# Kernel optimization log

Measured on AMD Instinct MI355X. Metric: run time of the kernel, lower is better.

Reference implementation:

```python
import jax, jax.numpy as jnp
import numpy as np

B, LQ, LT, LC = 256, 50, 12, 60
S = LQ + LT + LC
T = 80
D = 512   # gnn_hidden = lstm_hidden = att_vec_size
A = 128   # action_embed_size
FD = 64   # field_embed_size
TD = 64   # type_embed_size
NH = 8
DH = D // NH
NPROD, NFIELD, NTYPE = 96, 60, 30
IN_DIM = A + D + A + FD + TD + D  # prev_action|context|parent_prod|parent_field|parent_type|parent_state


def setup_inputs() -> dict:
    ks = jax.random.split(jax.random.key(0), 40)
    it = iter(range(40))
    def nrm(shape, scale=0.05):
        return jax.random.normal(ks[next(it)], shape, jnp.float32) * scale
    inp = {}
    inp["encodings"] = jax.random.normal(ks[next(it)], (B, S, D), jnp.float32)
    inp["mask"] = jnp.ones((B, S), dtype=bool)
    inp["h0"] = jax.random.normal(ks[next(it)], (B, D), jnp.float32)
    inp["act_type"] = jax.random.randint(ks[next(it)], (T, B), 0, 4)
    inp["act_idx"] = jax.random.randint(ks[next(it)], (T, B), 0, LT)
    inp["action_len"] = jax.random.randint(ks[next(it)], (B,), 1, T + 1)
    inp["parent_t"] = jax.random.randint(ks[next(it)], (T, B), 0, T)
    inp["frontier_prod"] = jax.random.randint(ks[next(it)], (T, B), 0, NPROD)
    inp["frontier_field"] = jax.random.randint(ks[next(it)], (T, B), 0, NFIELD)
    inp["frontier_type"] = jax.random.randint(ks[next(it)], (T, B), 0, NTYPE)
    inp["prod_embed"] = nrm((NPROD + 1, A))
    inp["field_embed"] = nrm((NFIELD, FD))
    inp["type_embed"] = nrm((NTYPE, TD))
    inp["col_in_W"] = nrm((D, A))
    inp["col_in_b"] = jnp.zeros((A,), jnp.float32)
    inp["lstm_Wi"] = nrm((IN_DIM, 4 * D))
    inp["lstm_Wh"] = nrm((D, 4 * D))
    inp["lstm_b"] = jnp.zeros((4 * D,), jnp.float32)
    for name in ("ctx", "colattn", "tabattn"):
        for w in ("Wq", "Wk", "Wv", "Wo"):
            inp[f"{name}_{w}"] = nrm((D, D))
    inp["att_W"] = nrm((2 * D, D))
    inp["att_b"] = jnp.zeros((D,), jnp.float32)
    inp["rule_W"] = nrm((D, A))
    return inp


def _mha(mem, m, q, Wq, Wk, Wv, Wo):
    # mem: [B,S,D] keys/values, q: [B,D] single-step query, m: [B,S] valid mask
    Sm = mem.shape[1]
    qh = (q @ Wq).reshape(B, NH, DH)
    kh = (mem @ Wk).reshape(B, Sm, NH, DH)
    vh = (mem @ Wv).reshape(B, Sm, NH, DH)
    scores = jnp.einsum('bhd,bshd->bhs', qh, kh) * (1.0 / float(np.sqrt(DH)))
    scores = jnp.where(m[:, None, :], scores, -1e9)
    p = jax.nn.softmax(scores, axis=-1)                  # [B,NH,S]
    ctx = jnp.einsum('bhs,bshd->bhd', p, vh).reshape(B, D) @ Wo
    return ctx, p.mean(axis=1)                           # context, head-avg attn prob


def forward(encodings, mask, h0, act_type, act_idx, action_len, parent_t,
            frontier_prod, frontier_field, frontier_type,
            prod_embed, field_embed, type_embed, col_in_W, col_in_b,
            lstm_Wi, lstm_Wh, lstm_b,
            ctx_Wq, ctx_Wk, ctx_Wv, ctx_Wo, att_W, att_b, rule_W,
            colattn_Wq, colattn_Wk, colattn_Wv, colattn_Wo,
            tabattn_Wq, tabattn_Wk, tabattn_Wv, tabattn_Wo):
    tab = encodings[:, LQ:LQ + LT]
    col = encodings[:, LQ + LT:]
    tab_mask = mask[:, LQ:LQ + LT]
    col_mask = mask[:, LQ + LT:]
    bidx = jnp.arange(B)

    def lstm_step(x, h, c):
        g = x @ lstm_Wi + h @ lstm_Wh + lstm_b
        i, f, gg, o = jnp.split(g, 4, axis=-1)
        c2 = jax.nn.sigmoid(f) * c + jax.nn.sigmoid(i) * jnp.tanh(gg)
        h2 = jax.nn.sigmoid(o) * jnp.tanh(c2)
        return h2, c2

    def decode_step(x, h, c):
        h2, c2 = lstm_step(x, h, c)
        ctx, _ = _mha(encodings, mask, h2, ctx_Wq, ctx_Wk, ctx_Wv, ctx_Wo)
        att = jnp.tanh(jnp.concatenate([h2, ctx], axis=-1) @ att_W + att_b)
        rule_lp = jax.nn.log_softmax((att @ rule_W) @ prod_embed.T, axis=-1)   # [B, NPROD+1]
        _, colp = _mha(col, col_mask, att, colattn_Wq, colattn_Wk, colattn_Wv, colattn_Wo)
        _, tabp = _mha(tab, tab_mask, att, tabattn_Wq, tabattn_Wk, tabattn_Wv, tabattn_Wo)
        return h2, c2, ctx, rule_lp, jnp.log(colp + 1e-32), jnp.log(tabp + 1e-32)

    def gather_lp(rule_lp, col_lp, tab_lp, atype, aidx):
        lp_rule = rule_lp[bidx, aidx]
        return jnp.where(atype == 0, lp_rule,
               jnp.where(atype == 1, rule_lp[:, NPROD],
               jnp.where(atype == 2, col_lp[bidx, aidx], tab_lp[bidx, aidx])))

    # ---- step t = 0: context from h0, zero input except context + root-type embed ----
    ctx0, _ = _mha(encodings, mask, h0, ctx_Wq, ctx_Wk, ctx_Wv, ctx_Wo)
    x0 = jnp.zeros((B, IN_DIM), encodings.dtype)
    x0 = x0.at[:, A:A + D].set(ctx0)
    off = A + D + A + FD
    x0 = x0.at[:, off:off + TD].set(jnp.broadcast_to(type_embed[0], (B, TD)))
    h, c, ctx, rule_lp, col_lp, tab_lp = decode_step(x0, h0, jnp.zeros_like(h0))
    lp0 = gather_lp(rule_lp, col_lp, tab_lp, act_type[0], act_idx[0])
    loss = jnp.sum(jnp.where(action_len > 0, lp0, 0.0))
    history = jnp.zeros((T, B, D), encodings.dtype).at[0].set(h)

    # ---- steps t = 1..T-1 ----
    def step(carry, xs):
        h, c, ctx, history, loss = carry
        t, ptype, pidx, atype, aidx, par, fp, ff, ft = xs
        valid = t < action_len                              # [B]
        # prev action embedding, gathered by heterogeneous action type
        pe_rule = prod_embed[jnp.where(ptype == 1, NPROD, pidx)]
        col_e = col[bidx, pidx] @ col_in_W + col_in_b
        tab_e = tab[bidx, pidx] @ col_in_W + col_in_b       # table_lstm_input shares weights
        prev = jnp.where((ptype <= 1)[:, None], pe_rule,
               jnp.where((ptype == 2)[:, None], col_e, tab_e))
        prev = jnp.where(valid[:, None], prev, 0.0)
        par_eff = jnp.where(valid, jnp.minimum(par, t - 1), 0)
        parent_state = history[par_eff, bidx]               # [B,D]
        x = jnp.concatenate([prev, ctx, prod_embed[fp], field_embed[ff],
                             type_embed[ft], parent_state], axis=-1)
        h, c, ctx, rule_lp, col_lp, tab_lp = decode_step(x, h, c)
        lp = gather_lp(rule_lp, col_lp, tab_lp, atype, aidx)
        loss = loss + jnp.sum(jnp.where(valid, lp, 0.0))
        history = jax.lax.dynamic_update_index_in_dim(history, h, t, 0)
        return (h, c, ctx, history, loss), None

    xs = (jnp.arange(1, T), act_type[:-1], act_idx[:-1], act_type[1:], act_idx[1:],
          parent_t[1:], frontier_prod[1:], frontier_field[1:], frontier_type[1:])
    (h, c, ctx, history, loss), _ = jax.lax.scan(step, (h, c, ctx, history, loss), xs)
    return -loss


def reference(encodings, mask, h0, act_type, act_idx, action_len, parent_t,
              frontier_prod, frontier_field, frontier_type,
              prod_embed, field_embed, type_embed, col_in_W, col_in_b,
              lstm_Wi, lstm_Wh, lstm_b,
              ctx_Wq, ctx_Wk, ctx_Wv, ctx_Wo, att_W, att_b, rule_W,
              colattn_Wq, colattn_Wk, colattn_Wv, colattn_Wo,
              tabattn_Wq, tabattn_Wk, tabattn_Wv, tabattn_Wo):
    return forward(encodings, mask, h0, act_type, act_idx, action_len, parent_t,
                   frontier_prod, frontier_field, frontier_type,
                   prod_embed, field_embed, type_embed, col_in_W, col_in_b,
                   lstm_Wi, lstm_Wh, lstm_b,
                   ctx_Wq, ctx_Wk, ctx_Wv, ctx_Wo, att_W, att_b, rule_W,
                   colattn_Wq, colattn_Wk, colattn_Wv, colattn_Wo,
                   tabattn_Wq, tabattn_Wk, tabattn_Wv, tabattn_Wo)
```

## Files before the change

### kernel.cpp

```cpp
#include <hip/hip_runtime.h>

typedef unsigned short u16;
typedef unsigned char u8;
typedef __attribute__((ext_vector_type(8))) short bf16x8;
typedef __attribute__((ext_vector_type(4))) float f32x4;
typedef __attribute__((ext_vector_type(2))) float f32x2;

#define NB   256
#define SEQ  122
#define TLT  12
#define TLC  60
#define NTT  80
#define DD   512
#define IND  1408
#define XHD  1920

__device__ __forceinline__ float bf2f(u16 u){ union{unsigned int i; float f;} x; x.i = ((unsigned int)u)<<16u; return x.f; }
__device__ __forceinline__ u16 f2bf(float f){ union{float f; unsigned int i;} x; x.f=f; unsigned int r = x.i + 0x7fffu + ((x.i>>16)&1u); return (u16)(r>>16); }

__device__ __forceinline__ void gstore(float* p, float v){ *p = v; }
__device__ __forceinline__ void gstore(u16* p, float v){ *p = f2bf(v); }

__global__ __launch_bounds__(256) void convert_bf16(const float* __restrict__ in, u16* __restrict__ out, int n){
    for (int i = blockIdx.x*256 + threadIdx.x; i < n; i += gridDim.x*256) out[i] = f2bf(in[i]);
// ... 43 lines not shown
    __shared__ float tile[64][65];
    int k0 = blockIdx.y*64, n0 = blockIdx.x*64;
    int c = threadIdx.x & 63, r4 = threadIdx.x >> 6;
    #pragma unroll
    for (int i = 0; i < 16; i++){
        int r = r4 + i*4;
        tile[r][c] = in[(size_t)(k0+r)*N + n0 + c];
    }
    __syncthreads();
    #pragma unroll
    for (int i = 0; i < 16; i++){
        int n = n0 + r4 + i*4;
        int pn = (n & 511)*4 + (n >> 9);
        out[(size_t)pn*ldo + koff + k0 + c] = f2bf(tile[c][r4 + i*4]);
    }
}

template<typename TOUT, int ACT>
__global__ __launch_bounds__(256) void gemm_kernel(
    const u16* __restrict__ Abase, int lda, int rpb, int sb, int aoff,
    const u16* __restrict__ BT,
    TOUT* __restrict__ C, int ldc,
    u16* __restrict__ C2, int ldc2,
    const float* __restrict__ bias, int K)
{
    __shared__ u16 As[64*40];
    __shared__ u16 Bs[64*40];
    const int bn = blockIdx.x * 64;
    const int bm = blockIdx.y * 64;
    const int tid = threadIdx.x, lane = tid & 63, wid = tid >> 6;
    const int wr = wid >> 1, wc = wid & 1;
    f32x4 acc[2][2];
    #pragma unroll
    for (int i=0;i<2;i++)
      #pragma unroll
      for (int j=0;j<2;j++) acc[i][j] = (f32x4){0.f,0.f,0.f,0.f};

    const int srow = tid >> 2, sseg = (tid & 3) << 3;
    int ar = bm + srow;
    int abr = (ar / rpb) * sb + aoff + (ar % rpb);
    const u16* ap = Abase + (size_t)abr * lda + sseg;
    const u16* bp = BT + (size_t)(bn + srow) * K + sseg;
    const int frow = lane & 15, fk = (lane >> 4) << 3;

    for (int k0 = 0; k0 < K; k0 += 32){
        uint4 av = *(const uint4*)(ap + k0);
        uint4 bv = *(const uint4*)(bp + k0);
        __syncthreads();
        *(uint4*)(&As[srow*40 + sseg]) = av;
        *(uint4*)(&Bs[srow*40 + sseg]) = bv;
        __syncthreads();
        #pragma unroll
        for (int i = 0; i < 2; i++){
            bf16x8 afr = *reinterpret_cast<const bf16x8*>(&As[(wr*32 + i*16 + frow)*40 + fk]);
            #pragma unroll
            for (int j = 0; j < 2; j++){
                bf16x8 bfr = *reinterpret_cast<const bf16x8*>(&Bs[(wc*32 + j*16 + frow)*40 + fk]);
                acc[i][j] = __builtin_amdgcn_mfma_f32_16x16x32_bf16(afr, bfr, acc[i][j], 0, 0, 0);
            }
        }
    }
    const int crow = (lane >> 4) * 4, ccol = lane & 15;
    #pragma unroll
    for (int i = 0; i < 2; i++){
        #pragma unroll
        for (int j = 0; j < 2; j++){
            int col = bn + wc*32 + j*16 + ccol;
            float bval = bias ? bias[col] : 0.0f;
            #pragma unroll
            for (int r = 0; r < 4; r++){
                int row = bm + wr*32 + i*16 + crow + r;
                float v = acc[i][j][r] + bval;
                if (ACT == 1) v = tanhf(v);
                gstore(&C[(size_t)row*ldc + col], v);
                if (C2) C2[(size_t)row*ldc2 + col] = f2bf(v);
            }
        }
    }
}

__global__ __launch_bounds__(256) void convert_h0(const float* __restrict__ h0, u16* __restrict__ hcP, u16* __restrict__ xh){
    int idx = blockIdx.x*256 + threadIdx.x;
    int b = idx >> 9, d = idx & 511;
    u16 hb = f2bf(h0[idx]);
    hcP[(size_t)b*1024 + d] = hb;
    xh[(size_t)b*XHD + IND + d] = hb;
}

__global__ __launch_bounds__(256) void build_x0(const float* __restrict__ typeE, u16* __restrict__ xh, float* __restrict__ cbuf){
    int b = blockIdx.x, tid = threadIdx.x;
    u16* xr = xh + (size_t)b*XHD;
    for (int j = tid; j < IND; j += 256){
        float v = (j >= 832 && j < 896) ? typeE[j-832] : 0.f;
        xr[j] = f2bf(v);
    }
    for (int j = tid; j < 512; j += 256) cbuf[(size_t)b*512 + j] = 0.f;
}

__global__ __launch_bounds__(256) void reduce_loss(const float* __restrict__ lp, float* __restrict__ out){
    __shared__ float sh[256];
    float s = 0.f;
    for (int i = threadIdx.x; i < NTT*NB; i += 256) s += lp[i];
    sh[threadIdx.x] = s; __syncthreads();
    for (int st = 128; st > 0; st >>= 1){ if (threadIdx.x < st) sh[threadIdx.x] += sh[threadIdx.x+st]; __syncthreads(); }
    if (threadIdx.x == 0) out[0] = -sh[0];
}


__device__ __forceinline__ void gemm64(const u16* __restrict__ A0, int lda,
                                       const u16* __restrict__ B0, int ldb,
                                       int K, u16* As, u16* Bs, f32x4 (&acc)[2][2])
{
    const int tid = threadIdx.x, lane = tid & 63;
    const int wid = tid >> 6, wr = wid >> 1, wc = wid & 1;
    const int frow = lane & 15, fk = (lane >> 4) << 3;
    const int srow = tid >> 2, sk = (tid & 3) << 4;
    const u16* ap = A0 + (size_t)srow * lda + sk;
    const u16* bp = B0 + (size_t)srow * ldb + sk;
    uint4 a0 = *(const uint4*)ap, a1 = *(const uint4*)(ap + 8);
    uint4 b0 = *(const uint4*)bp, b1 = *(const uint4*)(bp + 8);
    for (int k0 = 0; k0 < K; k0 += 64){
        __syncthreads();
        *(uint4*)&As[srow*72 + sk]     = a0;
        *(uint4*)&As[srow*72 + sk + 8] = a1;
        *(uint4*)&Bs[srow*72 + sk]     = b0;
        *(uint4*)&Bs[srow*72 + sk + 8] = b1;
        __syncthreads();
        if (k0 + 64 < K){
            ap += 64; bp += 64;
            a0 = *(const uint4*)ap; a1 = *(const uint4*)(ap + 8);
            b0 = *(const uint4*)bp; b1 = *(const uint4*)(bp + 8);
        }
        #pragma unroll
        for (int ks = 0; ks < 2; ks++){
            bf16x8 af0 = *(const bf16x8*)&As[(wr*32 + frow)*72      + ks*32 + fk];
            bf16x8 af1 = *(const bf16x8*)&As[(wr*32 + 16 + frow)*72 + ks*32 + fk];
            bf16x8 bf0 = *(const bf16x8*)&Bs[(wc*32 + frow)*72      + ks*32 + fk];
            bf16x8 bf1 = *(const bf16x8*)&Bs[(wc*32 + 16 + frow)*72 + ks*32 + fk];
            acc[0][0] = __builtin_amdgcn_mfma_f32_16x16x32_bf16(af0, bf0, acc[0][0], 0,0,0);
            acc[0][1] = __builtin_amdgcn_mfma_f32_16x16x32_bf16(af0, bf1, acc[0][1], 0,0,0);
            acc[1][0] = __builtin_amdgcn_mfma_f32_16x16x32_bf16(af1, bf0, acc[1][0], 0,0,0);
            acc[1][1] = __builtin_amdgcn_mfma_f32_16x16x32_bf16(af1, bf1, acc[1][1], 0,0,0);
        }
    }
}

__device__ __forceinline__ void zacc(f32x4 (&acc)[2][2]){
    #pragma unroll
    for (int i=0;i<2;i++)
      #pragma unroll
      for (int j=0;j<2;j++) acc[i][j] = (f32x4){0.f,0.f,0.f,0.f};
}

__global__ __launch_bounds__(256) void gates_lstm(
    int t, const u16* __restrict__ xh, const u16* __restrict__ WcatTp,
    const float* __restrict__ lb, float* __restrict__ cbuf,
    u16* __restrict__ hc)
{
    __shared__ union { struct { u16 A[2][32*72]; u16 B[2][32*72]; } g; float ep[32*33]; } sm;
    const int nt = blockIdx.x, mt = blockIdx.y;
    const int tid = threadIdx.x, lane = tid & 63, wid = tid >> 6;
    const int wr = wid >> 1, wc = wid & 1;
    const int frow = lane & 15, fk = (lane >> 4) << 3;
    const int crow = (lane >> 4) << 2, ccol = lane & 15;
    f32x4 acc = (f32x4){0.f,0.f,0.f,0.f};
    {
        const int srow = tid >> 2, sk = (tid & 3) << 4;
        const bool isA = srow < 32;
        const int drow = isA ? srow : srow - 32;
        const u16* p = isA ? (xh + (size_t)(mt*32 + srow)*XHD + sk)
                           : (WcatTp + (size_t)(nt*32 + (srow - 32))*XHD + sk);
        uint4 a0 = *(const uint4*)p, a1 = *(const uint4*)(p + 8);
        {
            u16* d = isA ? &sm.g.A[0][drow*72 + sk] : &sm.g.B[0][drow*72 + sk];
            *(uint4*)d = a0; *(uint4*)(d + 8) = a1;
        }
        __syncthreads();
        const int NIT = XHD/64;
        for (int i = 0; i < NIT; i++){
            if (i + 1 < NIT){
                p += 64;
                a0 = *(const uint4*)p; a1 = *(const uint4*)(p + 8);
            }
            const int cur = i & 1;
            #pragma unroll
            for (int ks = 0; ks < 2; ks++){
                bf16x8 af = *(const bf16x8*)&sm.g.A[cur][(wr*16 + frow)*72 + ks*32 + fk];
                bf16x8 bf = *(const bf16x8*)&sm.g.B[cur][(wc*16 + frow)*72 + ks*32 + fk];
                acc = __builtin_amdgcn_mfma_f32_16x16x32_bf16(af, bf, acc, 0,0,0);
            }
            if (i + 1 < NIT){
                u16* d = isA ? &sm.g.A[cur^1][drow*72 + sk] : &sm.g.B[cur^1][drow*72 + sk];
                *(uint4*)d = a0; *(uint4*)(d + 8) = a1;
                __syncthreads();
            }
        }
    }
    __syncthreads();
    #pragma unroll
    for (int r = 0; r < 4; r++)
        sm.ep[(wr*16 + crow + r)*33 + wc*16 + ccol] = acc[r];
    __syncthreads();
    {
        const int bloc = tid >> 3, dl = tid & 7;
        const int b = mt*32 + bloc, d = nt*8 + dl;
        float iv = sm.ep[bloc*33 + dl*4 + 0] + lb[d];
        float fv = sm.ep[bloc*33 + dl*4 + 1] + lb[512 + d];
        float gv = sm.ep[bloc*33 + dl*4 + 2] + lb[1024 + d];
        float ov = sm.ep[bloc*33 + dl*4 + 3] + lb[1536 + d];
        float c  = cbuf[(size_t)b*512 + d];
        float si = 1.f/(1.f + __expf(-iv));
        float sf = 1.f/(1.f + __expf(-fv));
        float so = 1.f/(1.f + __expf(-ov));
        float c2 = sf*c + si*tanhf(gv);
        float h2 = so*tanhf(c2);
        cbuf[(size_t)b*512 + d] = c2;
        hc[((size_t)t*NB + b)*1024 + d] = f2bf(h2);
    }
}

template<int ACT>
__global__ __launch_bounds__(256) void step_gemm(
    const u16* __restrict__ A0, int lda,
    const u16* __restrict__ BT, int ldb, int K,
    u16* __restrict__ C, int ldc, u16* __restrict__ C2, int ldc2,
    const float* __restrict__ bias)
{
    __shared__ u16 As[64*72];
    __shared__ u16 Bs[64*72];
    const int nt = blockIdx.x, mt = blockIdx.y;
    const int tid = threadIdx.x, lane = tid & 63, wid = tid >> 6;
    const int wr = wid >> 1, wc = wid & 1;
    const int crow = (lane >> 4) << 2, ccol = lane & 15;
    f32x4 acc[2][2]; zacc(acc);
    gemm64(A0 + (size_t)(mt*64)*lda, lda, BT + (size_t)(nt*64)*ldb, ldb, K, As, Bs, acc);
    #pragma unroll
    for (int i = 0; i < 2; i++)
      #pragma unroll
      for (int j = 0; j < 2; j++){
        int col = nt*64 + wc*32 + j*16 + ccol;
        float bv = bias ? bias[col] : 0.f;
        #pragma unroll
        for (int r = 0; r < 4; r++){
            int b = mt*64 + wr*32 + i*16 + crow + r;
            float v = acc[i][j][r] + bv;
            if (ACT == 1) v = tanhf(v);
            u16 hb = f2bf(v);
            C[(size_t)b*ldc + col] = hb;
            if (C2) C2[(size_t)b*ldc2 + col] = hb;
        }
      }
}

__device__ __forceinline__ float dot8(uint4 v, const float qv[8]){
    float a = 0.f;
    a += qv[0]*bf2f((u16)(v.x & 0xffffu)); a += qv[1]*bf2f((u16)(v.x >> 16));
    a += qv[2]*bf2f((u16)(v.y & 0xffffu)); a += qv[3]*bf2f((u16)(v.y >> 16));
    a += qv[4]*bf2f((u16)(v.z & 0xffffu)); a += qv[5]*bf2f((u16)(v.z >> 16));
    a += qv[6]*bf2f((u16)(v.w & 0xffffu)); a += qv[7]*bf2f((u16)(v.w >> 16));
    return a;
}

__device__ __forceinline__ float dot8f8(uint2 w, const float qv[8]){
    f32x2 a0 = __builtin_amdgcn_cvt_pk_f32_fp8((int)w.x, false);
    f32x2 a1 = __builtin_amdgcn_cvt_pk_f32_fp8((int)w.x, true);
    f32x2 a2 = __builtin_amdgcn_cvt_pk_f32_fp8((int)w.y, false);
    f32x2 a3 = __builtin_amdgcn_cvt_pk_f32_fp8((int)w.y, true);
    return qv[0]*a0.x + qv[1]*a0.y + qv[2]*a1.x + qv[3]*a1.y
         + qv[4]*a2.x + qv[5]*a2.y + qv[6]*a3.x + qv[7]*a3.y;
}
__device__ __forceinline__ void fma8f8(uint2 w, float pw, float a8[8]){
    f32x2 a0 = __builtin_amdgcn_cvt_pk_f32_fp8((int)w.x, false);
    f32x2 a1 = __builtin_amdgcn_cvt_pk_f32_fp8((int)w.x, true);
    f32x2 a2 = __builtin_amdgcn_cvt_pk_f32_fp8((int)w.y, false);
    f32x2 a3 = __builtin_amdgcn_cvt_pk_f32_fp8((int)w.y, true);
    a8[0] += pw*a0.x; a8[1] += pw*a0.y; a8[2] += pw*a1.x; a8[3] += pw*a1.y;
    a8[4] += pw*a2.x; a8[5] += pw*a2.y; a8[6] += pw*a3.x; a8[7] += pw*a3.y;
}

__global__ __launch_bounds__(512) void attnq_kernel(
    int t, const u16* __restrict__ WqTc, const u8* __restrict__ K8, const u8* __restrict__ V8,
    u16* __restrict__ hc_t, u16* __restrict__ xh,
    const u16* __restrict__ hc,
    const float* __restrict__ prodE, const float* __restrict__ fieldE, const float* __restrict__ typeE,
    const u16* __restrict__ cole, const u16* __restrict__ tabe,
    const int* __restrict__ act_type, const int* __restrict__ act_idx, const int* __restrict__ action_len,
    const int* __restrict__ parent_t, const int* __restrict__ f_prod, const int* __restrict__ f_field,
    const int* __restrict__ f_type)
{
    const int h = blockIdx.x, g = blockIdx.y;
    const int gb0 = g*8;
    const int tid = threadIdx.x;
    __shared__ u16 As2[2][16*72];
    __shared__ u16 Bs2[2][64*72];
    __shared__ float qs2[2][16*64];
    __shared__ float qs[16*64];
    __shared__ float sc[8*124];
    __shared__ float part[8*8*64];
    {
        const int kg = tid >> 8;
        const int lt = tid & 255;
        const int lane = lt & 63, wid4 = lt >> 6;
        const int frow = lane & 15, fk = (lane >> 4) << 3;
        f32x4 acc = (f32x4){0.f,0.f,0.f,0.f};
        const int srow = lt >> 2, sk = (lt & 3) << 4;
        const bool al = lt < 32;
        const u16* ap = hc_t + (size_t)(gb0 + srow)*1024 + kg*256 + sk;
        const u16* bp = WqTc + (size_t)(h*64 + srow)*512 + kg*256 + sk;
        u16* Ag = As2[kg]; u16* Bg = Bs2[kg];
        uint4 a0, a1, b0, b1;
        if (al){ a0 = *(const uint4*)ap; a1 = *(const uint4*)(ap + 8); }
        b0 = *(const uint4*)bp; b1 = *(const uint4*)(bp + 8);
        for (int k0 = 0; k0 < 256; k0 += 64){
            __syncthreads();
            if (al){ *(uint4*)&Ag[srow*72 + sk] = a0; *(uint4*)&Ag[srow*72 + sk + 8] = a1; }
            *(uint4*)&Bg[srow*72 + sk] = b0; *(uint4*)&Bg[srow*72 + sk + 8] = b1;
            __syncthreads();
            if (k0 + 64 < 256){
                bp += 64; b0 = *(const uint4*)bp; b1 = *(const uint4*)(bp + 8);
                if (al){ ap += 64; a0 = *(const uint4*)ap; a1 = *(const uint4*)(ap + 8); }
            }
            #pragma unroll
            for (int ks = 0; ks < 2; ks++){
                bf16x8 af = *(const bf16x8*)&Ag[frow*72 + ks*32 + fk];
                bf16x8 bf = *(const bf16x8*)&Bg[(wid4*16 + frow)*72 + ks*32 + fk];
                acc = __builtin_amdgcn_mfma_f32_16x16x32_bf16(af, bf, acc, 0,0,0);
            }
        }
        __syncthreads();
        #pragma unroll
        for (int r = 0; r < 4; r++)
            qs2[kg][((lane>>4)*4 + r)*64 + wid4*16 + (lane & 15)] = acc[r];
    }
    __syncthreads();
    for (int i = tid; i < 1024; i += 512)
        qs[i] = (qs2[0][i] + qs2[1][i]) * 0.125f;
    __syncthreads();
    {
        const int gi = tid >> 3, l8 = tid & 7;
        const int bq = gi & 7, sq = gi >> 3;
        float q8[8];
        const float* qrow = qs + bq*64 + l8*8;
        #pragma unroll
        for (int e = 0; e < 8; e++) q8[e] = qrow[e];
        const u8* Kb = K8 + ((size_t)(gb0 + bq)*SEQ)*512 + h*64 + l8*8;
        #pragma unroll 4
        for (int k = 0; k < 16; k++){
            int s = sq*16 + k;
            if (s < SEQ){
                uint2 kw = *(const uint2*)(Kb + (size_t)s*512);
                float a = dot8f8(kw, q8);
                a += __shfl_xor(a, 1); a += __shfl_xor(a, 2); a += __shfl_xor(a, 4);
                if (l8 == 0) sc[bq*124 + s] = a;
            }
        }
    }
    __syncthreads();
    {
        const int bq = tid >> 6, lid = tid & 63;
        float* scr = sc + bq*124;
        float m = -1e30f;
        for (int s = lid; s < SEQ; s += 64) m = fmaxf(m, scr[s]);
        #pragma unroll
        for (int mm = 1; mm < 64; mm <<= 1) m = fmaxf(m, __shfl_xor(m, mm));
        float sum = 0.f;
        for (int s = lid; s < SEQ; s += 64){ float e = __expf(scr[s] - m); scr[s] = e; sum += e; }
        #pragma unroll
        for (int mm = 1; mm < 64; mm <<= 1) sum += __shfl_xor(sum, mm);
        float inv = 1.f/sum;
        for (int s = lid; s < SEQ; s += 64) scr[s] *= inv;
    }
    __syncthreads();
    {
        const int gi = tid >> 3, l8 = tid & 7;
        const int bq = gi & 7, sq = gi >> 3;
        float a8[8] = {0.f,0.f,0.f,0.f,0.f,0.f,0.f,0.f};
        const u8* Vb = V8 + ((size_t)(gb0 + bq)*SEQ)*512 + h*64 + l8*8;
        const float* pr = sc + bq*124;
        #pragma unroll 4
        for (int k = 0; k < 16; k++){
            int s = sq*16 + k;
            if (s < SEQ){
                uint2 vw = *(const uint2*)(Vb + (size_t)s*512);
                fma8f8(vw, pr[s], a8);
            }
        }
        #pragma unroll
        for (int e = 0; e < 8; e++) part[(sq*8 + bq)*64 + l8*8 + e] = a8[e];
    }
    __syncthreads();
    if (tid < 256){
        const int bq = tid >> 5, d0 = (tid & 31)*2;
        float v0 = 0.f, v1 = 0.f;
        #pragma unroll
        for (int sq = 0; sq < 8; sq++){
            v0 += part[(sq*8 + bq)*64 + d0];
            v1 += part[(sq*8 + bq)*64 + d0 + 1];
        }
        unsigned outw = ((unsigned)f2bf(v1) << 16) | (unsigned)f2bf(v0);
        int b = gb0 + bq, c0 = h*64 + d0;
        *(unsigned*)(hc_t + (size_t)b*1024 + 512 + c0) = outw;
        *(unsigned*)(xh + (size_t)b*XHD + 128 + c0) = outw;
    }
    if (t >= 0 && t + 1 < NTT){
        int tn = t + 1;
        int b = gb0 + h;
        u16* xr = xh + (size_t)b*XHD;
        bool validn = tn < action_len[b];
        int ptype = act_type[t*NB + b], pidx = act_idx[t*NB + b];
        int fp = f_prod[tn*NB + b], ff = f_field[tn*NB + b], ftp = f_type[tn*NB + b];
        int par = parent_t[tn*NB + b];
        int pe = validn ? min(par, t) : 0;
        const u16* hrow  = hc + ((size_t)pe*NB + b)*1024;
        const u16* h2row = hc_t + (size_t)b*1024;
        if (tid < 256){
            unsigned v1 = *(const unsigned*)(hrow + tid*2);
            unsigned v2 = *(const unsigned*)(h2row + tid*2);
            *(unsigned*)(xr + 896 + tid*2)  = v1;
            *(unsigned*)(xr + 1408 + tid*2) = v2;
        } else if (tid < 384){
            int j = tid - 256;
            float v;
            if (!validn) v = 0.f;
            else if (ptype <= 1) v = prodE[(ptype == 1 ? 96 : pidx)*128 + j];
            else if (ptype == 2) v = bf2f(cole[((size_t)b*TLC + pidx)*128 + j]);
            else                 v = bf2f(tabe[((size_t)b*TLT + pidx)*128 + j]);
            xr[j] = f2bf(v);
            xr[640 + j] = f2bf(prodE[fp*128 + j]);
        } else if (tid < 448){
            int j = tid - 384;
            xr[768 + j] = f2bf(fieldE[ff*64 + j]);
            xr[832 + j] = f2bf(typeE[ftp*64 + j]);
        }
    }
}

__global__ __launch_bounds__(256) void tail_lp(
    const u16* __restrict__ rcq_all, const u16* __restrict__ Kcol, const u16* __restrict__ Ktab,
    const int* __restrict__ act_type, const int* __restrict__ act_idx, const int* __restrict__ action_len,
    float* __restrict__ lp_buf)
{
    const int t = blockIdx.x, b = blockIdx.y;
    const int tid = threadIdx.x;
    __shared__ float qc[512], qt[512];
    __shared__ float sccc[8*65];
    __shared__ float scct[8*17];
    __shared__ float lg[100];
    __shared__ float colv[64];
    __shared__ float tabv[16];
    __shared__ float red2[4];
    const u16* row = rcq_all + ((size_t)t*NB + b)*1152;
    if (tid < 97) lg[tid] = bf2f(row[tid]);
    {
        unsigned v = *(const unsigned*)(row + 128 + tid*2);
        qc[tid*2]   = bf2f((u16)(v & 0xffffu))*0.125f;
        qc[tid*2+1] = bf2f((u16)(v >> 16))*0.125f;
        unsigned v2 = *(const unsigned*)(row + 640 + tid*2);
        qt[tid*2]   = bf2f((u16)(v2 & 0xffffu))*0.125f;
        qt[tid*2+1] = bf2f((u16)(v2 >> 16))*0.125f;
    }
    __syncthreads();
    {
        const int gi = tid >> 3, l8 = tid & 7;
        for (int u = gi; u < 640; u += 32){
            if (u < 512){
                int hh = u >> 6, s = u & 63;
                if (s < TLC){
                    uint4 kv = *(const uint4*)(Kcol + ((size_t)b*TLC + s)*512 + hh*64 + l8*8);
                    float qv[8];
                    #pragma unroll
                    for (int e = 0; e < 8; e++) qv[e] = qc[hh*64 + l8*8 + e];
                    float a = dot8(kv, qv);
                    a += __shfl_xor(a, 1); a += __shfl_xor(a, 2); a += __shfl_xor(a, 4);
                    if (l8 == 0) sccc[hh*65 + s] = a;
                }
            } else {
                int v = u - 512, hh = v >> 4, s = v & 15;
                if (s < TLT){
                    uint4 kv = *(const uint4*)(Ktab + ((size_t)b*TLT + s)*512 + hh*64 + l8*8);
                    float qv[8];
                    #pragma unroll
                    for (int e = 0; e < 8; e++) qv[e] = qt[hh*64 + l8*8 + e];
                    float a = dot8(kv, qv);
                    a += __shfl_xor(a, 1); a += __shfl_xor(a, 2); a += __shfl_xor(a, 4);
                    if (l8 == 0) scct[hh*17 + s] = a;
                }
            }
        }
    }
    __syncthreads();
    {
        const int grp = tid >> 4, lid = tid & 15;
        if (grp < 8){
            float* scr = sccc + grp*65;
            float m = -1e30f;
            for (int s = lid; s < TLC; s += 16) m = fmaxf(m, scr[s]);
            #pragma unroll
            for (int mm = 1; mm < 16; mm <<= 1) m = fmaxf(m, __shfl_xor(m, mm));
            float sum = 0.f;
            for (int s = lid; s < TLC; s += 16){ float e = __expf(scr[s] - m); scr[s] = e; sum += e; }
            #pragma unroll
            for (int mm = 1; mm < 16; mm <<= 1) sum += __shfl_xor(sum, mm);
            float inv = 1.f/sum;
            for (int s = lid; s < TLC; s += 16) scr[s] *= inv;
        } else {
            float* scr = scct + (grp - 8)*17;
            float m = -1e30f;
            for (int s = lid; s < TLT; s += 16) m = fmaxf(m, scr[s]);
            #pragma unroll
            for (int mm = 1; mm < 16; mm <<= 1) m = fmaxf(m, __shfl_xor(m, mm));
            float sum = 0.f;
            for (int s = lid; s < TLT; s += 16){ float e = __expf(scr[s] - m); scr[s] = e; sum += e; }
            #pragma unroll
            for (int mm = 1; mm < 16; mm <<= 1) sum += __shfl_xor(sum, mm);
            float inv = 1.f/sum;
            for (int s = lid; s < TLT; s += 16) scr[s] *= inv;
        }
    }
    __syncthreads();
    if (tid < TLC){
        float a = 0.f;
        #pragma unroll
        for (int hh = 0; hh < 8; hh++) a += sccc[hh*65 + tid];
        colv[tid] = __logf(a*0.125f + 1e-32f);
    } else if (tid >= 64 && tid < 64 + TLT){
        int s = tid - 64;
        float a = 0.f;
        #pragma unroll
        for (int hh = 0; hh < 8; hh++) a += scct[hh*17 + s];
        tabv[s] = __logf(a*0.125f + 1e-32f);
    }
    if (tid < 128){
        float v = (tid < 97) ? lg[tid] : -1e30f;
        #pragma unroll
        for (int mm = 1; mm < 64; mm <<= 1) v = fmaxf(v, __shfl_xor(v, mm));
        if ((tid & 63) == 0) red2[tid >> 6] = v;
    }
    __syncthreads();
    {
        float M = fmaxf(red2[0], red2[1]);
        if (tid < 128){
            float e = (tid < 97) ? __expf(lg[tid] - M) : 0.f;
            #pragma unroll
            for (int mm = 1; mm < 64; mm <<= 1) e += __shfl_xor(e, mm);
            if ((tid & 63) == 0) red2[2 + (tid >> 6)] = e;
        }
        __syncthreads();
        if (tid == 0){
            float lse = M + __logf(red2[2] + red2[3]);
            int atype = act_type[t*NB + b], aidx = act_idx[t*NB + b];
            float lp = (atype == 0) ? (lg[aidx] - lse)
                     : (atype == 1) ? (lg[96] - lse)
                     : (atype == 2) ? colv[aidx] : tabv[aidx];
            lp_buf[t*NB + b] = (t < action_len[b]) ? lp : 0.f;
        }
    }
}

extern "C" void kernel_launch(void* const* d_in, const int* in_sizes, int n_in,
                              void* d_out, int out_size, void* d_ws, size_t ws_size,
                              hipStream_t stream)
{
    const float* encodings = (const float*)d_in[0];
    const float* h0        = (const float*)d_in[2];
    const int* act_type    = (const int*)d_in[3];
    const int* act_idx     = (const int*)d_in[4];
    const int* action_len  = (const int*)d_in[5];
    const int* parent_t    = (const int*)d_in[6];
    const int* f_prod      = (const int*)d_in[7];
    const int* f_field     = (const int*)d_in[8];
    const int* f_type      = (const int*)d_in[9];
    const float* prodE     = (const float*)d_in[10];
    const float* fieldE    = (const float*)d_in[11];
    const float* typeE     = (const float*)d_in[12];
    const float* col_in_W  = (const float*)d_in[13];
    const float* col_in_b  = (const float*)d_in[14];
    const float* lstm_Wi   = (const float*)d_in[15];
    const float* lstm_Wh   = (const float*)d_in[16];
    const float* lstm_b    = (const float*)d_in[17];
    const float* ctx_Wq    = (const float*)d_in[18];
    const float* ctx_Wk    = (const float*)d_in[19];
    const float* ctx_Wv    = (const float*)d_in[20];
    const float* ctx_Wo    = (const float*)d_in[21];
    const float* col_Wq    = (const float*)d_in[22];
    const float* col_Wk    = (const float*)d_in[23];
    const float* tab_Wq    = (const float*)d_in[26];
    const float* tab_Wk    = (const float*)d_in[27];
    const float* att_W     = (const float*)d_in[30];
    const float* att_b     = (const float*)d_in[31];
    const float* rule_W    = (const float*)d_in[32];

    char* w = (char*)d_ws;
    size_t off = 0;
    auto alloc = [&](size_t bytes)->char*{ char* pq = w + off; off = (off + bytes + 255) & ~(size_t)255; return pq; };

    u16* enc_bf  = (u16*)alloc((size_t)NB*SEQ*512*2);
    u16* WcatTp  = (u16*)alloc((size_t)2048*1920*2);
    u16* WqTc    = (u16*)alloc((size_t)512*512*2);
    u16* Wo_nt   = (u16*)alloc((size_t)512*512*2);
    u16* WkTc    = (u16*)alloc((size_t)512*512*2);
    u16* WvTc    = (u16*)alloc((size_t)512*512*2);
    u16* colWkT  = (u16*)alloc((size_t)512*512*2);
    u16* tabWkT  = (u16*)alloc((size_t)512*512*2);
    u16* colinWT = (u16*)alloc((size_t)128*512*2);
    u16* attWT   = (u16*)alloc((size_t)512*1024*2);
    u16* attW2T  = (u16*)alloc((size_t)512*1024*2);
    u16* Wfold   = (u16*)alloc((size_t)2048*512*2);
    u16* rcqT    = (u16*)alloc((size_t)1152*512*2);
    u16* prodEp  = (u16*)alloc((size_t)128*128*2);
    u16* ruleWb  = (u16*)alloc((size_t)512*128*2);
    u16* Kctx    = (u16*)alloc((size_t)NB*SEQ*512*2 + 16384);
    u16* Vctx    = (u16*)alloc((size_t)NB*SEQ*512*2 + 16384);
    u8*  K8      = (u8*)alloc((size_t)NB*SEQ*512);
    u8*  V8      = (u8*)alloc((size_t)NB*SEQ*512);
    u16* Kcol    = (u16*)alloc((size_t)NB*TLC*512*2);
    u16* Ktab    = (u16*)alloc((size_t)NB*TLT*512*2);
    u16* cole    = (u16*)alloc((size_t)NB*TLC*128*2);
    u16* tabe    = (u16*)alloc((size_t)NB*TLT*128*2);
    u16* hc      = (u16*)alloc((size_t)NTT*NB*1024*2);
    u16* hcP     = (u16*)alloc((size_t)NB*1024*2);
    u16* xh      = (u16*)alloc((size_t)NB*XHD*2);
    float* cbuf  = (float*)alloc((size_t)NB*512*4);
    float* lp_buf= (float*)alloc((size_t)NTT*NB*4);

    u16* attbuf_all = enc_bf;
    u16* rcq_all    = Kctx;

    const int IDENT = 1 << 30;

    convert_bf16<<<2048,256,0,stream>>>(encodings, enc_bf, NB*SEQ*512);
    convert_bf16<<<256,256,0,stream>>>(ctx_Wo, Wo_nt, 512*512);
    hipMemsetAsync(prodEp, 0, 128*128*2, stream);
    convert_bf16<<<64,256,0,stream>>>(prodE, prodEp, 97*128);
    convert_bf16<<<64,256,0,stream>>>(rule_W, ruleWb, 512*128);
    transpose_convert_perm<<<dim3(32,22),256,0,stream>>>(lstm_Wi, 1408, 2048, WcatTp, 1920, 0);
    transpose_convert_perm<<<dim3(32, 8),256,0,stream>>>(lstm_Wh,  512, 2048, WcatTp, 1920, 1408);
    transpose_convert<<<dim3(8,8),256,0,stream>>>(ctx_Wq, 512, 512, WqTc, 512, 0);
    transpose_convert<<<dim3(8,8),256,0,stream>>>(ctx_Wk, 512, 512, WkTc, 512, 0);
    transpose_convert<<<dim3(8,8),256,0,stream>>>(ctx_Wv, 512, 512, WvTc, 512, 0);
    transpose_convert<<<dim3(8,8),256,0,stream>>>(col_Wk, 512, 512, colWkT, 512, 0);
    transpose_convert<<<dim3(8,8),256,0,stream>>>(tab_Wk, 512, 512, tabWkT, 512, 0);
    transpose_convert<<<dim3(2,8),256,0,stream>>>(col_in_W, 512, 128, colinWT, 512, 0);
    transpose_convert<<<dim3(8,16),256,0,stream>>>(att_W, 1024, 512, attWT, 1024, 0);
    transpose_convert<<<dim3(8,8),256,0,stream>>>(col_Wq, 512, 512, rcqT + (size_t)128*512, 512, 0);
    transpose_convert<<<dim3(8,8),256,0,stream>>>(tab_Wq, 512, 512, rcqT + (size_t)640*512, 512, 0);

    gemm_kernel<u16,0><<<dim3(8,2),256,0,stream>>>(prodEp, 128, IDENT,0,0, ruleWb, rcqT, 512, nullptr,0, nullptr, 128);

    copy_u16<<<256,256,0,stream>>>(attWT, 1024, attW2T, 1024, 512*512, 9);
    gemm_kernel<u16,0><<<dim3(8,8),256,0,stream>>>(attWT+512, 1024, IDENT,0,0, Wo_nt, attW2T+512, 1024, nullptr,0, nullptr, 512);
    gemm_kernel<u16,0><<<dim3(8,32),256,0,stream>>>(WcatTp+128, 1920, IDENT,0,0, Wo_nt, Wfold, 512, nullptr,0, nullptr, 512);
    copy_u16<<<1024,256,0,stream>>>(Wfold, 512, WcatTp+128, 1920, 2048*512, 9);

    gemm_kernel<u16,0><<<dim3(8,488),256,0,stream>>>(enc_bf,512, IDENT,0,0,  WkTc,   Kctx,512, nullptr,0, nullptr, 512);
    gemm_kernel<u16,0><<<dim3(8,488),256,0,stream>>>(enc_bf,512, IDENT,0,0,  WvTc,   Vctx,512, nullptr,0, nullptr, 512);
    gemm_kernel<u16,0><<<dim3(8,240),256,0,stream>>>(enc_bf,512, 60,122,62,  colWkT, Kcol,512, nullptr,0, nullptr, 512);
    gemm_kernel<u16,0><<<dim3(8, 48),256,0,stream>>>(enc_bf,512, 12,122,50,  tabWkT, Ktab,512, nullptr,0, nullptr, 512);
    gemm_kernel<u16,0><<<dim3(2,240),256,0,stream>>>(enc_bf,512, 60,122,62,  colinWT,cole,128, nullptr,0, col_in_b, 512);
    gemm_kernel<u16,0><<<dim3(2, 48),256,0,stream>>>(enc_bf,512, 12,122,50,  colinWT,tabe,128, nullptr,0, col_in_b, 512);

    bf16_to_fp8<<<4096,256,0,stream>>>(Kctx, K8, NB*SEQ*512/4);
    bf16_to_fp8<<<4096,256,0,stream>>>(Vctx, V8, NB*SEQ*512/4);

    convert_h0<<<512,256,0,stream>>>(h0, hcP, xh);
    build_x0<<<NB,256,0,stream>>>(typeE, xh, cbuf);

    attnq_kernel<<<dim3(8,32),512,0,stream>>>(-1, WqTc, K8, V8, hcP, xh, hc,
                                              prodE, fieldE, typeE, cole, tabe,
                                              act_type, act_idx, action_len, parent_t, f_prod, f_field, f_type);

    for (int t = 0; t < NTT; t++){
        gates_lstm<<<dim3(64,8),256,0,stream>>>(t, xh, WcatTp, lstm_b, cbuf, hc);
        attnq_kernel<<<dim3(8,32),512,0,stream>>>(t, WqTc, K8, V8, hc + (size_t)t*NB*1024, xh, hc,
                                                  prodE, fieldE, typeE, cole, tabe,
                                                  act_type, act_idx, action_len, parent_t, f_prod, f_field, f_type);
    }

    step_gemm<1><<<dim3(8,320),256,0,stream>>>(hc, 1024, attW2T, 1024, 1024, attbuf_all, 512, nullptr, 0, att_b);
    step_gemm<0><<<dim3(18,320),256,0,stream>>>(attbuf_all, 512, rcqT, 512, 512, rcq_all, 1152, nullptr, 0, nullptr);
    tail_lp<<<dim3(NTT,NB),256,0,stream>>>(rcq_all, Kcol, Ktab, act_type, act_idx, action_len, lp_buf);

    reduce_loss<<<1,256,0,stream>>>(lp_buf, (float*)d_out);
}
```

Baseline: 3.780 ms.

## Replace per-step kernel launches with persistent decode kernel and grid barriers

Merges the 80-step loop of LSTM-gate and attention kernel launches into a single persistent kernel of 256 blocks. Each block runs two gate tiles per step and one attention head-group, and the phases are separated by a hierarchical atomic grid barrier. The aim is to remove roughly 160 kernel launches and their launch gaps. In exchange it adds barrier spin overhead, depends on all 256 blocks being co-resident (deadlock risk otherwise), and raises shared-memory use per block.

```diff
diff --git a/kernel.cpp b/kernel.cpp
--- a/kernel.cpp
+++ b/kernel.cpp
@@ -219,73 +219,6 @@
       for (int j=0;j<2;j++) acc[i][j] = (f32x4){0.f,0.f,0.f,0.f};
 }
 
-__global__ __launch_bounds__(256) void gates_lstm(
-    int t, const u16* __restrict__ xh, const u16* __restrict__ WcatTp,
-    const float* __restrict__ lb, float* __restrict__ cbuf,
-    u16* __restrict__ hc)
-{
-    __shared__ union { struct { u16 A[2][32*72]; u16 B[2][32*72]; } g; float ep[32*33]; } sm;
-    const int nt = blockIdx.x, mt = blockIdx.y;
-    const int tid = threadIdx.x, lane = tid & 63, wid = tid >> 6;
-    const int wr = wid >> 1, wc = wid & 1;
-    const int frow = lane & 15, fk = (lane >> 4) << 3;
-    const int crow = (lane >> 4) << 2, ccol = lane & 15;
-    f32x4 acc = (f32x4){0.f,0.f,0.f,0.f};
-    {
-        const int srow = tid >> 2, sk = (tid & 3) << 4;
-        const bool isA = srow < 32;
-        const int drow = isA ? srow : srow - 32;
-        const u16* p = isA ? (xh + (size_t)(mt*32 + srow)*XHD + sk)
-                           : (WcatTp + (size_t)(nt*32 + (srow - 32))*XHD + sk);
-        uint4 a0 = *(const uint4*)p, a1 = *(const uint4*)(p + 8);
-        {
-            u16* d = isA ? &sm.g.A[0][drow*72 + sk] : &sm.g.B[0][drow*72 + sk];
-            *(uint4*)d = a0; *(uint4*)(d + 8) = a1;
-        }
-        __syncthreads();
-        const int NIT = XHD/64;
-        for (int i = 0; i < NIT; i++){
-            if (i + 1 < NIT){
-                p += 64;
-                a0 = *(const uint4*)p; a1 = *(const uint4*)(p + 8);
-            }
-            const int cur = i & 1;
-            #pragma unroll
-            for (int ks = 0; ks < 2; ks++){
-                bf16x8 af = *(const bf16x8*)&sm.g.A[cur][(wr*16 + frow)*72 + ks*32 + fk];
-                bf16x8 bf = *(const bf16x8*)&sm.g.B[cur][(wc*16 + frow)*72 + ks*32 + fk];
-                acc = __builtin_amdgcn_mfma_f32_16x16x32_bf16(af, bf, acc, 0,0,0);
-            }
-            if (i + 1 < NIT){
-                u16* d = isA ? &sm.g.A[cur^1][drow*72 + sk] : &sm.g.B[cur^1][drow*72 + sk];
-                *(uint4*)d = a0; *(uint4*)(d + 8) = a1;
-                __syncthreads();
-            }
-        }
-    }
-    __syncthreads();
-    #pragma unroll
-    for (int r = 0; r < 4; r++)
-        sm.ep[(wr*16 + crow + r)*33 + wc*16 + ccol] = acc[r];
-    __syncthreads();
-    {
-        const int bloc = tid >> 3, dl = tid & 7;
-        const int b = mt*32 + bloc, d = nt*8 + dl;
-        float iv = sm.ep[bloc*33 + dl*4 + 0] + lb[d];
-        float fv = sm.ep[bloc*33 + dl*4 + 1] + lb[512 + d];
-        float gv = sm.ep[bloc*33 + dl*4 + 2] + lb[1024 + d];
-        float ov = sm.ep[bloc*33 + dl*4 + 3] + lb[1536 + d];
-        float c  = cbuf[(size_t)b*512 + d];
-        float si = 1.f/(1.f + __expf(-iv));
-        float sf = 1.f/(1.f + __expf(-fv));
-        float so = 1.f/(1.f + __expf(-ov));
-        float c2 = sf*c + si*tanhf(gv);
-        float h2 = so*tanhf(c2);
-        cbuf[(size_t)b*512 + d] = c2;
-        hc[((size_t)t*NB + b)*1024 + d] = f2bf(h2);
-    }
-}
-
 template<int ACT>
 __global__ __launch_bounds__(256) void step_gemm(
     const u16* __restrict__ A0, int lda,
@@ -327,7 +260,6 @@
     a += qv[6]*bf2f((u16)(v.w & 0xffffu)); a += qv[7]*bf2f((u16)(v.w >> 16));
     return a;
 }
-
 __device__ __forceinline__ float dot8f8(uint2 w, const float qv[8]){
     f32x2 a0 = __builtin_amdgcn_cvt_pk_f32_fp8((int)w.x, false);
     f32x2 a1 = __builtin_amdgcn_cvt_pk_f32_fp8((int)w.x, true);
@@ -345,15 +277,268 @@
     a8[4] += pw*a2.x; a8[5] += pw*a2.y; a8[6] += pw*a3.x; a8[7] += pw*a3.y;
 }
 
-__global__ __launch_bounds__(512) void attnq_kernel(
-    int t, const u16* __restrict__ WqTc, const u8* __restrict__ K8, const u8* __restrict__ V8,
-    u16* __restrict__ hc_t, u16* __restrict__ xh,
-    const u16* __restrict__ hc,
+union SMP {
+    struct {
+        struct { u16 A[2][32*72]; u16 B[2][32*72]; } t[2];
+        float ep[2][32*33];
+    } g;
+    struct {
+        u16 As2[2][16*72];
+        u16 Bs2[2][64*72];
+        float qs2[2][16*64];
+        float qs[16*64];
+        float sc[8*124];
+        float part[8*8*64];
+    } a;
+};
+
+__device__ __forceinline__ void gridbar(int* barw, int gen){
+    __syncthreads();
+    if (threadIdx.x == 0){
+        __builtin_amdgcn_fence(__ATOMIC_RELEASE, "agent");
+        int g = blockIdx.x & 7;
+        int prev = __hip_atomic_fetch_add(&barw[16*g], 1, __ATOMIC_RELAXED, __HIP_MEMORY_SCOPE_AGENT);
+        if (prev == gen*32 - 1){
+            int pr = __hip_atomic_fetch_add(&barw[16*8], 1, __ATOMIC_RELAXED, __HIP_MEMORY_SCOPE_AGENT);
+            if (pr == gen*8 - 1)
+                __hip_atomic_store(&barw[16*9], gen, __ATOMIC_RELEASE, __HIP_MEMORY_SCOPE_AGENT);
+        }
+        while (__hip_atomic_load(&barw[16*9], __ATOMIC_RELAXED, __HIP_MEMORY_SCOPE_AGENT) < gen)
+            __builtin_amdgcn_s_sleep(4);
+        __builtin_amdgcn_fence(__ATOMIC_ACQUIRE, "agent");
+    }
+    __syncthreads();
+}
+
+__global__ __launch_bounds__(512) void decode_persist(
+    u16* __restrict__ xh, const u16* __restrict__ WcatTp,
+    const float* __restrict__ lb, float* __restrict__ cbuf, u16* __restrict__ hc,
+    const u16* __restrict__ WqTc, const u8* __restrict__ K8, const u8* __restrict__ V8,
     const float* __restrict__ prodE, const float* __restrict__ fieldE, const float* __restrict__ typeE,
     const u16* __restrict__ cole, const u16* __restrict__ tabe,
     const int* __restrict__ act_type, const int* __restrict__ act_idx, const int* __restrict__ action_len,
     const int* __restrict__ parent_t, const int* __restrict__ f_prod, const int* __restrict__ f_field,
-    const int* __restrict__ f_type)
+    const int* __restrict__ f_type, int* __restrict__ barw)
+{
+    __shared__ SMP sm;
+    const int tid = threadIdx.x;
+    const int bid = blockIdx.x;
+    int gen = 0;
+
+    for (int t = 0; t < NTT; t++){
+        u16* hc_t = hc + (size_t)t*NB*1024;
+        {
+            const int sub = tid >> 8;
+            const int lt = tid & 255;
+            const int tau = bid*2 + sub;
+            const int nt = tau >> 3, mt = tau & 7;
+            const int lane = lt & 63, wid = lt >> 6;
+            const int wr = wid >> 1, wc = wid & 1;
+            const int frow = lane & 15, fk = (lane >> 4) << 3;
+            const int crow = (lane >> 4) << 2, ccol = lane & 15;
+            f32x4 acc = (f32x4){0.f,0.f,0.f,0.f};
+            {
+                const int srow = lt >> 2, sk = (lt & 3) << 4;
+                const bool isA = srow < 32;
+                const int drow = isA ? srow : srow - 32;
+                const u16* p = isA ? (xh + (size_t)(mt*32 + srow)*XHD + sk)
+                                   : (WcatTp + (size_t)(nt*32 + (srow - 32))*XHD + sk);
+                uint4 a0 = *(const uint4*)p, a1 = *(const uint4*)(p + 8);
+                {
+                    u16* d = isA ? &sm.g.t[sub].A[0][drow*72 + sk] : &sm.g.t[sub].B[0][drow*72 + sk];
+                    *(uint4*)d = a0; *(uint4*)(d + 8) = a1;
+                }
+                __syncthreads();
+                const int NIT = XHD/64;
+                for (int i = 0; i < NIT; i++){
+                    if (i + 1 < NIT){
+                        p += 64;
+                        a0 = *(const uint4*)p; a1 = *(const uint4*)(p + 8);
+                    }
+                    const int cur = i & 1;
+                    #pragma unroll
+                    for (int ks = 0; ks < 2; ks++){
+                        bf16x8 af = *(const bf16x8*)&sm.g.t[sub].A[cur][(wr*16 + frow)*72 + ks*32 + fk];
+                        bf16x8 bf = *(const bf16x8*)&sm.g.t[sub].B[cur][(wc*16 + frow)*72 + ks*32 + fk];
+                        acc = __builtin_amdgcn_mfma_f32_16x16x32_bf16(af, bf, acc, 0,0,0);
+                    }
+                    if (i + 1 < NIT){
+                        u16* d = isA ? &sm.g.t[sub].A[cur^1][drow*72 + sk] : &sm.g.t[sub].B[cur^1][drow*72 + sk];
+                        *(uint4*)d = a0; *(uint4*)(d + 8) = a1;
+                        __syncthreads();
+                    }
+                }
+            }
+            __syncthreads();
+            #pragma unroll
+            for (int r = 0; r < 4; r++)
+                sm.g.ep[sub][(wr*16 + crow + r)*33 + wc*16 + ccol] = acc[r];
+            __syncthreads();
+            {
+                const int bloc = lt >> 3, dl = lt & 7;
+                const int b = mt*32 + bloc, d = nt*8 + dl;
+                float iv = sm.g.ep[sub][bloc*33 + dl*4 + 0] + lb[d];
+                float fv = sm.g.ep[sub][bloc*33 + dl*4 + 1] + lb[512 + d];
+                float gv = sm.g.ep[sub][bloc*33 + dl*4 + 2] + lb[1024 + d];
+                float ov = sm.g.ep[sub][bloc*33 + dl*4 + 3] + lb[1536 + d];
+                float c  = cbuf[(size_t)b*512 + d];
+                float si = 1.f/(1.f + __expf(-iv));
+                float sf = 1.f/(1.f + __expf(-fv));
+                float so = 1.f/(1.f + __expf(-ov));
+                float c2 = sf*c + si*tanhf(gv);
+                float h2 = so*tanhf(c2);
+                cbuf[(size_t)b*512 + d] = c2;
+                hc_t[(size_t)b*1024 + d] = f2bf(h2);
+            }
+        }
+        gen++; gridbar(barw, gen);
+        {
+            const int h = bid & 7, g = bid >> 3;
+            const int gb0 = g*8;
+            {
+                const int kg = tid >> 8;
+                const int lt = tid & 255;
+                const int lane = lt & 63, wid4 = lt >> 6;
+                const int frow = lane & 15, fk = (lane >> 4) << 3;
+                f32x4 acc = (f32x4){0.f,0.f,0.f,0.f};
+                const int srow = lt >> 2, sk = (lt & 3) << 4;
+                const bool al = lt < 32;
+                const u16* ap = hc_t + (size_t)(gb0 + srow)*1024 + kg*256 + sk;
+                const u16* bp = WqTc + (size_t)(h*64 + srow)*512 + kg*256 + sk;
+                u16* Ag = sm.a.As2[kg]; u16* Bg = sm.a.Bs2[kg];
+                uint4 a0, a1, b0, b1;
+                if (al){ a0 = *(const uint4*)ap; a1 = *(const uint4*)(ap + 8); }
+                b0 = *(const uint4*)bp; b1 = *(const uint4*)(bp + 8);
+                for (int k0 = 0; k0 < 256; k0 += 64){
+                    __syncthreads();
+                    if (al){ *(uint4*)&Ag[srow*72 + sk] = a0; *(uint4*)&Ag[srow*72 + sk + 8] = a1; }
+                    *(uint4*)&Bg[srow*72 + sk] = b0; *(uint4*)&Bg[srow*72 + sk + 8] = b1;
+                    __syncthreads();
+                    if (k0 + 64 < 256){
+                        bp += 64; b0 = *(const uint4*)bp; b1 = *(const uint4*)(bp + 8);
+                        if (al){ ap += 64; a0 = *(const uint4*)ap; a1 = *(const uint4*)(ap + 8); }
+                    }
+                    #pragma unroll
+                    for (int ks = 0; ks < 2; ks++){
+                        bf16x8 af = *(const bf16x8*)&Ag[frow*72 + ks*32 + fk];
+                        bf16x8 bf = *(const bf16x8*)&Bg[(wid4*16 + frow)*72 + ks*32 + fk];
+                        acc = __builtin_amdgcn_mfma_f32_16x16x32_bf16(af, bf, acc, 0,0,0);
+                    }
+                }
+                __syncthreads();
+                #pragma unroll
+                for (int r = 0; r < 4; r++)
+                    sm.a.qs2[kg][((lane>>4)*4 + r)*64 + wid4*16 + (lane & 15)] = acc[r];
+            }
+            __syncthreads();
+            for (int i = tid; i < 1024; i += 512)
+                sm.a.qs[i] = (sm.a.qs2[0][i] + sm.a.qs2[1][i]) * 0.125f;
+            __syncthreads();
+            {
+                const int gi = tid >> 3, l8 = tid & 7;
+                const int bq = gi & 7, sq = gi >> 3;
+                float q8[8];
+                const float* qrow = sm.a.qs + bq*64 + l8*8;
+                #pragma unroll
+                for (int e = 0; e < 8; e++) q8[e] = qrow[e];
+                const u8* Kb = K8 + ((size_t)(gb0 + bq)*SEQ)*512 + h*64 + l8*8;
+                #pragma unroll 4
+                for (int k = 0; k < 16; k++){
+                    int s = sq*16 + k;
+                    if (s < SEQ){
+                        uint2 kw = *(const uint2*)(Kb + (size_t)s*512);
+                        float a = dot8f8(kw, q8);
+                        a += __shfl_xor(a, 1); a += __shfl_xor(a, 2); a += __shfl_xor(a, 4);
+                        if (l8 == 0) sm.a.sc[bq*124 + s] = a;
+                    }
+                }
+            }
+            __syncthreads();
+            {
+                const int bq = tid >> 6, lid = tid & 63;
+                float* scr = sm.a.sc + bq*124;
+                float m = -1e30f;
+                for (int s = lid; s < SEQ; s += 64) m = fmaxf(m, scr[s]);
+                #pragma unroll
+                for (int mm = 1; mm < 64; mm <<= 1) m = fmaxf(m, __shfl_xor(m, mm));
+                float sum = 0.f;
+                for (int s = lid; s < SEQ; s += 64){ float e = __expf(scr[s] - m); scr[s] = e; sum += e; }
+                #pragma unroll
+                for (int mm = 1; mm < 64; mm <<= 1) sum += __shfl_xor(sum, mm);
+                float inv = 1.f/sum;
+                for (int s = lid; s < SEQ; s += 64) scr[s] *= inv;
+            }
+            __syncthreads();
+            {
+                const int gi = tid >> 3, l8 = tid & 7;
+                const int bq = gi & 7, sq = gi >> 3;
+                float a8[8] = {0.f,0.f,0.f,0.f,0.f,0.f,0.f,0.f};
+                const u8* Vb = V8 + ((size_t)(gb0 + bq)*SEQ)*512 + h*64 + l8*8;
+                const float* pr = sm.a.sc + bq*124;
+                #pragma unroll 4
+                for (int k = 0; k < 16; k++){
+                    int s = sq*16 + k;
+                    if (s < SEQ){
+                        uint2 vw = *(const uint2*)(Vb + (size_t)s*512);
+                        fma8f8(vw, pr[s], a8);
+                    }
+                }
+                #pragma unroll
+                for (int e = 0; e < 8; e++) sm.a.part[(sq*8 + bq)*64 + l8*8 + e] = a8[e];
+            }
+            __syncthreads();
+            if (tid < 256){
+                const int bq = tid >> 5, d0 = (tid & 31)*2;
+                float v0 = 0.f, v1 = 0.f;
+                #pragma unroll
+                for (int sq = 0; sq < 8; sq++){
+                    v0 += sm.a.part[(sq*8 + bq)*64 + d0];
+                    v1 += sm.a.part[(sq*8 + bq)*64 + d0 + 1];
+                }
+                unsigned outw = ((unsigned)f2bf(v1) << 16) | (unsigned)f2bf(v0);
+                int b = gb0 + bq, c0 = h*64 + d0;
+                *(unsigned*)(hc_t + (size_t)b*1024 + 512 + c0) = outw;
+                *(unsigned*)(xh + (size_t)b*XHD + 128 + c0) = outw;
+            }
+            if (t + 1 < NTT){
+                int tn = t + 1;
+                int b = gb0 + h;
+                u16* xr = xh + (size_t)b*XHD;
+                bool validn = tn < action_len[b];
+                int ptype = act_type[t*NB + b], pidx = act_idx[t*NB + b];
+                int fp = f_prod[tn*NB + b], ff = f_field[tn*NB + b], ftp = f_type[tn*NB + b];
+                int par = parent_t[tn*NB + b];
+                int pe = validn ? min(par, t) : 0;
+                const u16* hrow  = hc + ((size_t)pe*NB + b)*1024;
+                const u16* h2row = hc_t + (size_t)b*1024;
+                if (tid < 256){
+                    unsigned v1 = *(const unsigned*)(hrow + tid*2);
+                    unsigned v2 = *(const unsigned*)(h2row + tid*2);
+                    *(unsigned*)(xr + 896 + tid*2)  = v1;
+                    *(unsigned*)(xr + 1408 + tid*2) = v2;
+                } else if (tid < 384){
+                    int j = tid - 256;
+                    float v;
+                    if (!validn) v = 0.f;
+                    else if (ptype <= 1) v = prodE[(ptype == 1 ? 96 : pidx)*128 + j];
+                    else if (ptype == 2) v = bf2f(cole[((size_t)b*TLC + pidx)*128 + j]);
+                    else                 v = bf2f(tabe[((size_t)b*TLT + pidx)*128 + j]);
+                    xr[j] = f2bf(v);
+                    xr[640 + j] = f2bf(prodE[fp*128 + j]);
+                } else if (tid < 448){
+                    int j = tid - 384;
+                    xr[768 + j] = f2bf(fieldE[ff*64 + j]);
+                    xr[832 + j] = f2bf(typeE[ftp*64 + j]);
+                }
+            }
+        }
+        gen++; gridbar(barw, gen);
+    }
+}
+
+__global__ __launch_bounds__(512) void attnq_kernel(
+    const u16* __restrict__ WqTc, const u8* __restrict__ K8, const u8* __restrict__ V8,
+    u16* __restrict__ hc_t, u16* __restrict__ xh)
 {
     const int h = blockIdx.x, g = blockIdx.y;
     const int gb0 = g*8;
@@ -469,37 +654,6 @@
         *(unsigned*)(hc_t + (size_t)b*1024 + 512 + c0) = outw;
         *(unsigned*)(xh + (size_t)b*XHD + 128 + c0) = outw;
     }
-    if (t >= 0 && t + 1 < NTT){
-        int tn = t + 1;
-        int b = gb0 + h;
-        u16* xr = xh + (size_t)b*XHD;
-        bool validn = tn < action_len[b];
-        int ptype = act_type[t*NB + b], pidx = act_idx[t*NB + b];
-        int fp = f_prod[tn*NB + b], ff = f_field[tn*NB + b], ftp = f_type[tn*NB + b];
-        int par = parent_t[tn*NB + b];
-        int pe = validn ? min(par, t) : 0;
-        const u16* hrow  = hc + ((size_t)pe*NB + b)*1024;
-        const u16* h2row = hc_t + (size_t)b*1024;
-        if (tid < 256){
-            unsigned v1 = *(const unsigned*)(hrow + tid*2);
-            unsigned v2 = *(const unsigned*)(h2row + tid*2);
-            *(unsigned*)(xr + 896 + tid*2)  = v1;
-            *(unsigned*)(xr + 1408 + tid*2) = v2;
-        } else if (tid < 384){
-            int j = tid - 256;
-            float v;
-            if (!validn) v = 0.f;
-            else if (ptype <= 1) v = prodE[(ptype == 1 ? 96 : pidx)*128 + j];
-            else if (ptype == 2) v = bf2f(cole[((size_t)b*TLC + pidx)*128 + j]);
-            else                 v = bf2f(tabe[((size_t)b*TLT + pidx)*128 + j]);
-            xr[j] = f2bf(v);
-            xr[640 + j] = f2bf(prodE[fp*128 + j]);
-        } else if (tid < 448){
-            int j = tid - 384;
-            xr[768 + j] = f2bf(fieldE[ff*64 + j]);
-            xr[832 + j] = f2bf(typeE[ftp*64 + j]);
-        }
-    }
 }
 
 __global__ __launch_bounds__(256) void tail_lp(
@@ -661,6 +815,7 @@
     size_t off = 0;
     auto alloc = [&](size_t bytes)->char*{ char* pq = w + off; off = (off + bytes + 255) & ~(size_t)255; return pq; };
 
+    int* barw    = (int*)alloc(1024);
     u16* enc_bf  = (u16*)alloc((size_t)NB*SEQ*512*2);
     u16* WcatTp  = (u16*)alloc((size_t)2048*1920*2);
     u16* WqTc    = (u16*)alloc((size_t)512*512*2);
@@ -695,6 +850,8 @@
 
     const int IDENT = 1 << 30;
 
+    hipMemsetAsync(barw, 0, 1024, stream);
+
     convert_bf16<<<2048,256,0,stream>>>(encodings, enc_bf, NB*SEQ*512);
     convert_bf16<<<256,256,0,stream>>>(ctx_Wo, Wo_nt, 512*512);
     hipMemsetAsync(prodEp, 0, 128*128*2, stream);
@@ -732,16 +889,12 @@
     convert_h0<<<512,256,0,stream>>>(h0, hcP, xh);
     build_x0<<<NB,256,0,stream>>>(typeE, xh, cbuf);
 
-    attnq_kernel<<<dim3(8,32),512,0,stream>>>(-1, WqTc, K8, V8, hcP, xh, hc,
-                                              prodE, fieldE, typeE, cole, tabe,
-                                              act_type, act_idx, action_len, parent_t, f_prod, f_field, f_type);
-
-    for (int t = 0; t < NTT; t++){
-        gates_lstm<<<dim3(64,8),256,0,stream>>>(t, xh, WcatTp, lstm_b, cbuf, hc);
-        attnq_kernel<<<dim3(8,32),512,0,stream>>>(t, WqTc, K8, V8, hc + (size_t)t*NB*1024, xh, hc,
-                                                  prodE, fieldE, typeE, cole, tabe,
-                                                  act_type, act_idx, action_len, parent_t, f_prod, f_field, f_type);
-    }
+    attnq_kernel<<<dim3(8,32),512,0,stream>>>(WqTc, K8, V8, hcP, xh);
+
+    decode_persist<<<256,512,0,stream>>>(xh, WcatTp, lstm_b, cbuf, hc, WqTc, K8, V8,
+                                         prodE, fieldE, typeE, cole, tabe,
+                                         act_type, act_idx, action_len, parent_t,
+                                         f_prod, f_field, f_type, barw);
 
     step_gemm<1><<<dim3(8,320),256,0,stream>>>(hc, 1024, attW2T, 1024, 1024, attbuf_all, 512, nullptr, 0, att_b);
     step_gemm<0><<<dim3(18,320),256,0,stream>>>(attbuf_all, 512, rcqT, 512, 512, rcq_all, 1152, nullptr, 0, nullptr);
```

After: 4.918 ms. 1.3x slower.
